# Kernel tuning notes

Measured on AMD Instinct MI355X. Metric: run time of the kernel, lower is better.

The kernel has to match this reference:

```python
import jax, jax.numpy as jnp
import numpy as np

B = 4096
NUM_USERS = 100000
H_DIM = 128          # HIDDEN_DIM
IN_DIM = 128 + 8 + 32  # BOARD_FEAT_DIM + ACTION_BITS + USER_EMB_DIM


def _conv(x, w, b):
    # x: [B,C,H,W], w: [O,I,3,3] (torch OIHW), padding=1 -> SAME
    y = jax.lax.conv_general_dilated(
        x, w, window_strides=(1, 1), padding='SAME',
        dimension_numbers=('NCHW', 'OIHW', 'NCHW'))
    return y + b[None, :, None, None]


def _maxpool2(x):
    return jax.lax.reduce_window(x, -jnp.inf, jax.lax.max,
                                 (1, 1, 2, 2), (1, 1, 2, 2), 'VALID')


def setup_inputs() -> dict:
    key = jax.random.key(0)
    ks = jax.random.split(key, 24)
    f32 = jnp.float32

    def n(k, shape, s=0.05):
        return jax.random.normal(k, shape, dtype=f32) * s

    return {
        'board': jax.random.uniform(ks[0], (B, 1, 32, 32), dtype=f32),
        'h': jax.random.normal(ks[1], (1, B, H_DIM), dtype=f32),
        'action_token': jax.random.randint(ks[2], (B,), 0, 256, dtype=jnp.int32),
        'user_idx': jax.random.randint(ks[3], (B,), 0, NUM_USERS, dtype=jnp.int32),
        # SmallBoardCNN params
        'conv1_w': n(ks[4], (16, 1, 3, 3)), 'conv1_b': n(ks[5], (16,)),
        'conv2_w': n(ks[6], (32, 16, 3, 3)), 'conv2_b': n(ks[7], (32,)),
        'conv3_w': n(ks[8], (64, 32, 3, 3)), 'conv3_b': n(ks[9], (64,)),
        'conv4_w': n(ks[10], (128, 64, 3, 3)), 'conv4_b': n(ks[11], (128,)),
        'proj_w': n(ks[12], (128, 128)), 'proj_b': n(ks[13], (128,)),
        # user embedding
        'emb': n(ks[14], (NUM_USERS, 32), 1.0),
        # GRU params (torch layout: [3H, in], gate order r,z,n)
        'w_ih': n(ks[15], (3 * H_DIM, IN_DIM)), 'w_hh': n(ks[16], (3 * H_DIM, H_DIM)),
        'b_ih': n(ks[17], (3 * H_DIM,)), 'b_hh': n(ks[18], (3 * H_DIM,)),
        # head
        'head_w': n(ks[19], (6, H_DIM)), 'head_b': n(ks[20], (6,)),
    }


def reference(board, h, action_token, user_idx,
              conv1_w, conv1_b, conv2_w, conv2_b, conv3_w, conv3_b,
              conv4_w, conv4_b, proj_w, proj_b, emb,
              w_ih, w_hh, b_ih, b_hh, head_w, head_b):
    # SmallBoardCNN
    x = jax.nn.relu(_conv(board, conv1_w, conv1_b))
    x = jax.nn.relu(_conv(x, conv2_w, conv2_b))
    x = _maxpool2(x)                       # [B,32,16,16]
    x = jax.nn.relu(_conv(x, conv3_w, conv3_b))
    x = _maxpool2(x)                       # [B,64,8,8]
    x = jax.nn.relu(_conv(x, conv4_w, conv4_b))
    bf = x.mean(axis=(2, 3)) @ proj_w.T + proj_b   # AdaptiveAvgPool(1,1) + Linear -> [B,128]

    # int_to_8bits, batched
    abits = ((action_token[:, None] >> jnp.arange(8)) & 1).astype(jnp.float32)  # [B,8]
    uemb = emb[user_idx]                              # [B,32]
    xin = jnp.concatenate([bf, abits, uemb], axis=1)  # [B,168]

    # single GRU step (torch GRUCell math, gate order r,z,n)
    h0 = h[0]                                         # [B,128]
    gi = xin @ w_ih.T + b_ih                          # [B,384]
    gh = h0 @ w_hh.T + b_hh
    r = jax.nn.sigmoid(gi[:, :H_DIM] + gh[:, :H_DIM])
    z = jax.nn.sigmoid(gi[:, H_DIM:2 * H_DIM] + gh[:, H_DIM:2 * H_DIM])
    n_ = jnp.tanh(gi[:, 2 * H_DIM:] + r * gh[:, 2 * H_DIM:])
    h_new = (1.0 - z) * n_ + z * h0                   # [B,128]

    logits = h_new @ head_w.T + head_b                # [B,6]
    return logits, h_new[None]                        # h_new: [1,B,128]
```

## Files before the change

### kernel.cpp

```cpp
#include <hip/hip_runtime.h>
#include <hip/hip_bf16.h>

#define BATCH 4096

typedef __attribute__((ext_vector_type(8))) short short8;
typedef __attribute__((ext_vector_type(16))) float f32x16;

#define WB1_ELEM 0
#define WB2_ELEM 512
#define WB3_ELEM 5120
#define WB4_ELEM 23552
#define WB_TOTAL 97280

#define A1_OFF 2320
#define ZS1_OFF 35088
#define A2_OFF 35152
#define ZS2_OFF 51536
#define SMEM_F 51600
#define ZS3_REL 8192
#define MEANV_OFF 8320

static __device__ __forceinline__ unsigned pack2(float a, float b) {
    __hip_bfloat16 lo = __float2bfloat16(a), hi = __float2bfloat16(b);
    unsigned short ul = *(unsigned short*)&lo, uh = *(unsigned short*)&hi;
    return ((unsigned)uh << 16) | ul;
}

static __device__ __forceinline__ void store_bf16(void* p, float v) {
    __hip_bfloat16 b = __float2bfloat16(v);
    *(unsigned short*)p = *(unsigned short*)&b;
}

__global__ void prepack_weights(const float* __restrict__ w1,
                                const float* __restrict__ w2,
                                const float* __restrict__ w3,
                                const float* __restrict__ w4,
                                __hip_bfloat16* __restrict__ wb) {
    int g = blockIdx.x * 256 + threadIdx.x;
    if (g < 512) {
        int oc = g >> 4, k = g & 15;
        float v = (oc < 16 && k < 9) ? w1[oc * 9 + k] : 0.f;
        wb[g] = __float2bfloat16(v);
    } else if (g < WB3_ELEM) {
        int gg = g - WB2_ELEM;
        int oc = gg / 144, r = gg - oc * 144, tap = r >> 4, ic = r & 15;
        wb[g] = __float2bfloat16(w2[oc * 144 + ic * 9 + tap]);
    } else if (g < WB4_ELEM) {
        int gg = g - WB3_ELEM;
        int oc = gg / 288, r = gg - oc * 288, tap = r >> 5, ic = r & 31;
        wb[g] = __float2bfloat16(w3[oc * 288 + ic * 9 + tap]);
    } else if (g < WB_TOTAL) {
        int gg = g - WB4_ELEM;
        int oc = gg / 576, r = gg - oc * 576, tap = r >> 6, ic = r & 63;
        wb[g] = __float2bfloat16(w4[oc * 576 + ic * 9 + tap]);
    }
}

__global__ __launch_bounds__(256, 3) void cnn_fused_kernel(
    const float* __restrict__ board,
    const float* __restrict__ b1, const float* __restrict__ b2,
    const float* __restrict__ b3, const float* __restrict__ b4,
    const float* __restrict__ pw, const float* __restrict__ pb,
    const __hip_bfloat16* __restrict__ wb,
    float* __restrict__ bf_out)
{
    __shared__ alignas(16) char smem[SMEM_F];
    unsigned short* sbu = (unsigned short*)smem;
    char* a1b = smem + A1_OFF;
    char* a3b = smem;
    float* meanv = (float*)(smem + MEANV_OFF);

    const int t = threadIdx.x;
    const int img = blockIdx.x;
    const int w = t >> 6;
    const int l = t & 63;
    const int n = l & 31;
    const int h = l >> 5;

    const char* wb3 = (const char*)(wb + WB3_ELEM);
    const char* wb4 = (const char*)(wb + WB4_ELEM);

    {
        for (int i = t; i < 132; i += 256) {
            int row, col;
            if (i < 34)       { row = 0;  col = i; }
            else if (i < 68)  { row = 33; col = i - 34; }
            else if (i < 100) { row = i - 68 + 1;  col = 0; }
            else              { row = i - 100 + 1; col = 33; }
            sbu[row * 34 + col] = 0;
        }
        uint4 z; z.x = z.y = z.z = z.w = 0u;
        if (t < 4) ((uint4*)(smem + ZS1_OFF))[t] = z;
        else if (t >= 4 && t < 8) ((uint4*)(smem + ZS2_OFF))[t - 4] = z;
    }
    __syncthreads();

    {
        float4 v = ((const float4*)board)[img * 256 + t];
        const int p0 = t * 4;
        const int row = (p0 >> 5) + 1, col = (p0 & 31) + 1;
        unsigned short* d = sbu + row * 34 + col;
        __hip_bfloat16 x0 = __float2bfloat16(v.x), x1 = __float2bfloat16(v.y);
        __hip_bfloat16 x2 = __float2bfloat16(v.z), x3 = __float2bfloat16(v.w);
        d[0] = *(unsigned short*)&x0; d[1] = *(unsigned short*)&x1;
        d[2] = *(unsigned short*)&x2; d[3] = *(unsigned short*)&x3;
    }
    __syncthreads();

    {
        const short8 A1 = *(const short8*)((const char*)wb + (n * 16 + h * 8) * 2);
        float b1s[8];
#pragma unroll
        for (int r = 0; r < 8; ++r) b1s[r] = b1[(r & 3) + 8 * (r >> 2) + 4 * h];
        const unsigned* sbw = (const unsigned*)smem;
#pragma unroll 1
        for (int yi = 0; yi < 8; ++yi) {
            const int y = 8 * w + yi;
            unsigned short c[3][3];
#pragma unroll
            for (int dy = 0; dy < 3; ++dy) {
                const int base = (y + dy) * 17 + (n >> 1);
                const unsigned w0 = sbw[base], w1v = sbw[base + 1];
                if (n & 1) {
                    c[dy][0] = (unsigned short)(w0 >> 16);
                    c[dy][1] = (unsigned short)(w1v & 0xffff);
                    c[dy][2] = (unsigned short)(w1v >> 16);
                } else {
                    c[dy][0] = (unsigned short)(w0 & 0xffff);
                    c[dy][1] = (unsigned short)(w0 >> 16);
                    c[dy][2] = (unsigned short)(w1v & 0xffff);
                }
            }
            short8 Bv;
            if (h == 0) {
                Bv[0] = (short)c[0][0]; Bv[1] = (short)c[0][1]; Bv[2] = (short)c[0][2];
                Bv[3] = (short)c[1][0]; Bv[4] = (short)c[1][1]; Bv[5] = (short)c[1][2];
                Bv[6] = (short)c[2][0]; Bv[7] = (short)c[2][1];
            } else {
                Bv = (short8)0;
                Bv[0] = (short)c[2][2];
            }
            f32x16 acc = __builtin_amdgcn_mfma_f32_32x32x16_bf16(A1, Bv, (f32x16)0.0f, 0, 0, 0);
            float v8[8];
#pragma unroll
            for (int r = 0; r < 8; ++r) v8[r] = fmaxf(acc[r] + b1s[r], 0.f);
            const int key = ((n >> 2) & 1) << 4;
            char* dst = a1b + (y * 32 + n) * 32;
            uint2 u0, u1;
            u0.x = pack2(v8[0], v8[1]); u0.y = pack2(v8[2], v8[3]);
            u1.x = pack2(v8[4], v8[5]); u1.y = pack2(v8[6], v8[7]);
            *(uint2*)(dst + ((h * 8) ^ key)) = u0;
            *(uint2*)(dst + ((h * 8 + 16) ^ key)) = u1;
        }
    }
    __syncthreads();

    {
        const char* wb2 = (const char*)(wb + WB2_ELEM);
        short8 Bw[9];
#pragma unroll
        for (int tp = 0; tp < 9; ++tp)
            Bw[tp] = *(const short8*)(wb2 + (n * 144 + tp * 16 + h * 8) * 2);
        const float biasv = b2[n];
        const int y_off = 2 * ((n >> 2) & 1) + ((n >> 1) & 1);
        const int x_off = 2 * ((n >> 3) & 3) + (n & 1);

#pragma unroll 1
        for (int pp = 0; pp < 2; ++pp) {
            const int py_base = 4 * w + 2 * pp;
            const int yb = 2 * py_base + y_off;
#pragma unroll 1
            for (int pxh = 0; pxh < 2; ++pxh) {
                const int x0 = 16 * pxh + x_off;
                f32x16 acc0 = (f32x16)0.0f, acc1 = (f32x16)0.0f;
#pragma unroll
                for (int tp = 0; tp < 9; ++tp) {
                    const int dy = tp / 3, dx = tp - 3 * dy;
                    const int r_u = yb + dy - 1;
                    const int c0 = x0 + dx - 1, c1 = x0 + 8 + dx - 1;
                    const bool okr = (unsigned)r_u < 32u;
                    const int off0 = (okr && (unsigned)c0 < 32u)
                        ? (A1_OFF + (r_u * 32 + c0) * 32 + ((h * 16) ^ (((c0 >> 2) & 1) << 4)))
                        : (ZS1_OFF + h * 16);
                    const int off1 = (okr && (unsigned)c1 < 32u)
                        ? (A1_OFF + (r_u * 32 + c1) * 32 + ((h * 16) ^ (((c1 >> 2) & 1) << 4)))
                        : (ZS1_OFF + h * 16);
                    short8 A0 = *(const short8*)(smem + off0);
                    short8 A1v = *(const short8*)(smem + off1);
                    acc0 = __builtin_amdgcn_mfma_f32_32x32x16_bf16(A0, Bw[tp], acc0, 0, 0, 0);
                    acc1 = __builtin_amdgcn_mfma_f32_32x32x16_bf16(A1v, Bw[tp], acc1, 0, 0, 0);
                }
                const int py = py_base + h;
#pragma unroll
                for (int e = 0; e < 2; ++e) {
                    const f32x16 acc = e ? acc1 : acc0;
                    const int pxb = 2 * pxh + e;
#pragma unroll
                    for (int j = 0; j < 4; ++j) {
                        float v = fmaxf(fmaxf(acc[4 * j], acc[4 * j + 1]),
                                        fmaxf(acc[4 * j + 2], acc[4 * j + 3]));
                        v = fmaxf(v + biasv, 0.f);
                        const int px = 4 * pxb + j;
                        const int key = (py + 2 * px) & 3;
                        store_bf16(smem + A2_OFF + (py * 16 + px) * 64 +
                                   ((((n >> 3) ^ key) & 3) << 4) + ((n * 2) & 15), v);
                    }
                }
            }
        }
    }
    __syncthreads();

    {
        uint4 z; z.x = z.y = z.z = z.w = 0u;
        if (t < 8) ((uint4*)(a3b + ZS3_REL))[t] = z;
    }
    __syncthreads();

    {
        const int y_off = 2 * ((n >> 2) & 1) + ((n >> 1) & 1);
        const int x_off = 2 * ((n >> 3) & 3) + (n & 1);
        const int y_in = 4 * w + y_off;
        f32x16 acc00 = (f32x16)0.0f, acc01 = (f32x16)0.0f;
        f32x16 acc10 = (f32x16)0.0f, acc11 = (f32x16)0.0f;
#pragma unroll
        for (int step = 0; step < 18; ++step) {
            const int tp = step >> 1, kh = step & 1;
            const int dy = tp / 3, dx = tp - 3 * dy;
            short8 B0 = *(const short8*)(wb3 + ((n)      * 288 + tp * 32 + kh * 16 + h * 8) * 2);
            short8 B1 = *(const short8*)(wb3 + ((32 + n) * 288 + tp * 32 + kh * 16 + h * 8) * 2);
            const int row_u = y_in + dy - 1;
            const int col0 = x_off + dx - 1;
            const int col1 = col0 + 8;
            const int sbase = kh * 32 + h * 16;
            const bool okr = (unsigned)row_u < 16u;
            const int off0 = (okr && (unsigned)col0 < 16u)
                ? (A2_OFF + row_u * 1024 + col0 * 64 + (sbase ^ (((row_u + 2 * col0) & 3) << 4)))
                : (ZS2_OFF + sbase);
            const int off1 = (okr && (unsigned)col1 < 16u)
                ? (A2_OFF + row_u * 1024 + col1 * 64 + (sbase ^ (((row_u + 2 * col1) & 3) << 4)))
                : (ZS2_OFF + sbase);
            short8 A0 = *(const short8*)(smem + off0);
            short8 A1v = *(const short8*)(smem + off1);
            acc00 = __builtin_amdgcn_mfma_f32_32x32x16_bf16(A0, B0, acc00, 0, 0, 0);
            acc01 = __builtin_amdgcn_mfma_f32_32x32x16_bf16(A0, B1, acc01, 0, 0, 0);
            acc10 = __builtin_amdgcn_mfma_f32_32x32x16_bf16(A1v, B0, acc10, 0, 0, 0);
            acc11 = __builtin_amdgcn_mfma_f32_32x32x16_bf16(A1v, B1, acc11, 0, 0, 0);
        }
        const int py = 2 * w + h;
#pragma unroll
        for (int e = 0; e < 4; ++e) {
            const f32x16 acc = (e == 0) ? acc00 : (e == 1) ? acc01 : (e == 2) ? acc10 : acc11;
            const int pxb = e >> 1, ocb = e & 1;
            const float biasv = b3[32 * ocb + n];
#pragma unroll
            for (int j = 0; j < 4; ++j) {
                float v = fmaxf(fmaxf(acc[4 * j], acc[4 * j + 1]),
                                fmaxf(acc[4 * j + 2], acc[4 * j + 3]));
                v = fmaxf(v + biasv, 0.f);
                const int px = 4 * pxb + j;
                const int byte_in = ocb * 64 + n * 2;
                const int key3 = (py + 2 * px) & 7;
                store_bf16(a3b + (py * 8 + px) * 128 +
                           ((((byte_in >> 4) ^ key3) << 4) | (byte_in & 15)), v);
            }
        }
    }
    __syncthreads();

    {
        const int x4 = n & 7, y4 = (n >> 3) & 3;
        f32x16 aE0 = (f32x16)0.0f, aO0 = (f32x16)0.0f;
        f32x16 aE1 = (f32x16)0.0f, aO1 = (f32x16)0.0f;
#pragma unroll
        for (int dy = 0; dy < 3; ++dy)
#pragma unroll
            for (int dx = 0; dx < 3; ++dx) {
                const int row0 = y4 + dy - 1;
                const int col_u = x4 + dx - 1;
                const bool okc = (unsigned)col_u < 8u;
                const bool ok0 = okc && ((unsigned)row0 < 8u);
                const bool ok1 = okc && ((unsigned)(row0 + 4) < 8u);
#pragma unroll
                for (int kc = 0; kc < 4; ++kc) {
                    const int s4 = kc * 32 + h * 16;
                    const int off0 = ok0
                        ? ((row0 * 8 + col_u) * 128 + (s4 ^ (((row0 + 2 * col_u) & 7) << 4)))
                        : (ZS3_REL + s4);
                    const int off1 = ok1
                        ? (((row0 + 4) * 8 + col_u) * 128 + (s4 ^ (((row0 + 4 + 2 * col_u) & 7) << 4)))
                        : (ZS3_REL + s4);
                    short8 B = *(const short8*)(wb4 + ((32 * w + n) * 576 + (dy * 3 + dx) * 64 + kc * 16 + h * 8) * 2);
                    short8 A0 = *(const short8*)(a3b + off0);
                    short8 A1v = *(const short8*)(a3b + off1);
                    if (kc & 1) {
                        aO0 = __builtin_amdgcn_mfma_f32_32x32x16_bf16(A0, B, aO0, 0, 0, 0);
                        aO1 = __builtin_amdgcn_mfma_f32_32x32x16_bf16(A1v, B, aO1, 0, 0, 0);
                    } else {
                        aE0 = __builtin_amdgcn_mfma_f32_32x32x16_bf16(A0, B, aE0, 0, 0, 0);
                        aE1 = __builtin_amdgcn_mfma_f32_32x32x16_bf16(A1v, B, aE1, 0, 0, 0);
                    }
                }
            }
        const float biasv = b4[32 * w + n];
        float s = 0.f;
#pragma unroll
        for (int r = 0; r < 16; ++r) {
            s += fmaxf(aE0[r] + aO0[r] + biasv, 0.f);
            s += fmaxf(aE1[r] + aO1[r] + biasv, 0.f);
        }
        s += __shfl_xor(s, 32);
        if (l < 32) meanv[32 * w + l] = s * (1.f / 64.f);
    }
    __syncthreads();

    if (t < 128) {
        float acc = pb[t];
        const float* wrow = pw + t * 128;
        for (int k = 0; k < 128; ++k) acc = fmaf(meanv[k], wrow[k], acc);
        bf_out[img * 128 + t] = acc;
    }
}

__global__ __launch_bounds__(384) void gru_kernel(
    const float* __restrict__ hin,
    const int* __restrict__ atok, const int* __restrict__ uidx,
    const float* __restrict__ emb,
    const float* __restrict__ w_ih, const float* __restrict__ w_hh,
    const float* __restrict__ b_ih, const float* __restrict__ b_hh,
    const float* __restrict__ head_w, const float* __restrict__ head_b,
    float* __restrict__ out)
{
    const int img0 = blockIdx.x * 8;
    const int t = threadIdx.x;
    __shared__ float xin_s[8][168];
    __shared__ float h0_s[8][128];
    __shared__ float gis[8][384];
    __shared__ float ghs[8][384];
    __shared__ float hn_s[8][128];
    const float* bf = out + BATCH * 6;

    for (int idx = t; idx < 8 * 168; idx += 384) {
        const int r = idx / 168, k = idx - r * 168;
        const int row = img0 + r;
        float v;
        if (k < 128)      v = bf[row * 128 + k];
        else if (k < 136) v = (float)((atok[row] >> (k - 128)) & 1);
        else              v = emb[uidx[row] * 32 + (k - 136)];
        xin_s[r][k] = v;
    }
    for (int idx = t; idx < 8 * 128; idx += 384) {
        const int r = idx >> 7, k = idx & 127;
        h0_s[r][k] = hin[(img0 + r) * 128 + k];
    }
    __syncthreads();

    {
        const int o = t;
        float gi[8], gh[8];
        const float bi = b_ih[o], bh = b_hh[o];
#pragma unroll
        for (int r = 0; r < 8; ++r) { gi[r] = bi; gh[r] = bh; }
        const float* wi = w_ih + o * 168;
        const float* wh = w_hh + o * 128;
        for (int k = 0; k < 128; ++k) {
            const float wv = wi[k];
            const float wvh = wh[k];
#pragma unroll
            for (int r = 0; r < 8; ++r) {
                gi[r] = fmaf(wv, xin_s[r][k], gi[r]);
                gh[r] = fmaf(wvh, h0_s[r][k], gh[r]);
            }
        }
        for (int k = 128; k < 168; ++k) {
            const float wv = wi[k];
#pragma unroll
            for (int r = 0; r < 8; ++r) gi[r] = fmaf(wv, xin_s[r][k], gi[r]);
        }
#pragma unroll
        for (int r = 0; r < 8; ++r) { gis[r][o] = gi[r]; ghs[r][o] = gh[r]; }
    }
    __syncthreads();

    if (t < 128) {
#pragma unroll
        for (int r = 0; r < 8; ++r) {
            const float rg = 1.f / (1.f + expf(-(gis[r][t] + ghs[r][t])));
            const float z  = 1.f / (1.f + expf(-(gis[r][128 + t] + ghs[r][128 + t])));
            const float nn = tanhf(gis[r][256 + t] + rg * ghs[r][256 + t]);
            const float hn = (1.f - z) * nn + z * h0_s[r][t];
            hn_s[r][t] = hn;
            out[BATCH * 6 + (img0 + r) * 128 + t] = hn;
        }
    }
    __syncthreads();

    if (t < 48) {
        const int r = t / 6, j = t - r * 6;
        float acc = head_b[j];
        const float* wrow = head_w + j * 128;
        for (int k = 0; k < 128; ++k) acc = fmaf(hn_s[r][k], wrow[k], acc);
        out[(img0 + r) * 6 + j] = acc;
    }
}

extern "C" void kernel_launch(void* const* d_in, const int* in_sizes, int n_in,
                              void* d_out, int out_size, void* d_ws, size_t ws_size,
                              hipStream_t stream) {
    const float* board = (const float*)d_in[0];
    const float* h     = (const float*)d_in[1];
    const int*   atok  = (const int*)d_in[2];
    const int*   uidx  = (const int*)d_in[3];
    const float* w1 = (const float*)d_in[4];
    const float* b1 = (const float*)d_in[5];
    const float* w2 = (const float*)d_in[6];
    const float* b2 = (const float*)d_in[7];
    const float* w3 = (const float*)d_in[8];
    const float* b3 = (const float*)d_in[9];
    const float* w4 = (const float*)d_in[10];
    const float* b4 = (const float*)d_in[11];
    const float* pw = (const float*)d_in[12];
    const float* pb = (const float*)d_in[13];
    const float* emb  = (const float*)d_in[14];
    const float* w_ih = (const float*)d_in[15];
    const float* w_hh = (const float*)d_in[16];
    const float* b_ih = (const float*)d_in[17];
    const float* b_hh = (const float*)d_in[18];
    const float* head_w = (const float*)d_in[19];
    const float* head_b = (const float*)d_in[20];
    float* out = (float*)d_out;
    __hip_bfloat16* wb = (__hip_bfloat16*)d_ws;

    float* bf = out + BATCH * 6;
    prepack_weights<<<(WB_TOTAL + 255) / 256, 256, 0, stream>>>(w1, w2, w3, w4, wb);
    cnn_fused_kernel<<<BATCH, 256, 0, stream>>>(board, b1, b2, b3, b4,
                                                pw, pb, wb, bf);
    gru_kernel<<<BATCH / 8, 384, 0, stream>>>(h, atok, uidx, emb, w_ih, w_hh,
                                              b_ih, b_hh, head_w, head_b, out);
}
```

Baseline: 213.8 us.

## Double CNN block to 512 threads and split conv work across eight waves

The fused CNN kernel now runs 512 threads (8 waves) per image instead of 256. Each conv stage is repartitioned so every wave does half the previous work: conv1 rows, conv2 pooled rows, conv3 split by pixel half, and conv4 split by row half with partial means combined in shared memory. The projection dot product is split across two threads per output and joined with a shuffle. The goal is more waves to hide latency and a shorter serial chain per wave. The cost is fewer accumulators per wave and lost register reuse: conv2 weights are now reloaded inside the loop, and conv3/conv4 A/B fragments are no longer shared across two MFMAs. The 512x6 launch bounds also tighten the register budget.

```diff
diff --git a/kernel.cpp b/kernel.cpp
--- a/kernel.cpp
+++ b/kernel.cpp
@@ -19,6 +19,7 @@
 #define SMEM_F 51600
 #define ZS3_REL 8192
 #define MEANV_OFF 8320
+#define MEANP_OFF 8832
 
 static __device__ __forceinline__ unsigned pack2(float a, float b) {
     __hip_bfloat16 lo = __float2bfloat16(a), hi = __float2bfloat16(b);
@@ -56,7 +57,7 @@
     }
 }
 
-__global__ __launch_bounds__(256, 3) void cnn_fused_kernel(
+__global__ __launch_bounds__(512, 6) void cnn_fused_kernel(
     const float* __restrict__ board,
     const float* __restrict__ b1, const float* __restrict__ b2,
     const float* __restrict__ b3, const float* __restrict__ b4,
@@ -69,6 +70,7 @@
     char* a1b = smem + A1_OFF;
     char* a3b = smem;
     float* meanv = (float*)(smem + MEANV_OFF);
+    float* meanp = (float*)(smem + MEANP_OFF);
 
     const int t = threadIdx.x;
     const int img = blockIdx.x;
@@ -81,8 +83,8 @@
     const char* wb4 = (const char*)(wb + WB4_ELEM);
 
     {
-        for (int i = t; i < 132; i += 256) {
-            int row, col;
+        if (t < 132) {
+            int i = t, row, col;
             if (i < 34)       { row = 0;  col = i; }
             else if (i < 68)  { row = 33; col = i - 34; }
             else if (i < 100) { row = i - 68 + 1;  col = 0; }
@@ -90,20 +92,18 @@
             sbu[row * 34 + col] = 0;
         }
         uint4 z; z.x = z.y = z.z = z.w = 0u;
-        if (t < 4) ((uint4*)(smem + ZS1_OFF))[t] = z;
-        else if (t >= 4 && t < 8) ((uint4*)(smem + ZS2_OFF))[t - 4] = z;
-    }
-    __syncthreads();
-
-    {
-        float4 v = ((const float4*)board)[img * 256 + t];
-        const int p0 = t * 4;
+        if (t >= 256 && t < 260) ((uint4*)(smem + ZS1_OFF))[t - 256] = z;
+        else if (t >= 260 && t < 264) ((uint4*)(smem + ZS2_OFF))[t - 260] = z;
+    }
+    __syncthreads();
+
+    {
+        float2 v = ((const float2*)board)[img * 512 + t];
+        const int p0 = t * 2;
         const int row = (p0 >> 5) + 1, col = (p0 & 31) + 1;
         unsigned short* d = sbu + row * 34 + col;
         __hip_bfloat16 x0 = __float2bfloat16(v.x), x1 = __float2bfloat16(v.y);
-        __hip_bfloat16 x2 = __float2bfloat16(v.z), x3 = __float2bfloat16(v.w);
         d[0] = *(unsigned short*)&x0; d[1] = *(unsigned short*)&x1;
-        d[2] = *(unsigned short*)&x2; d[3] = *(unsigned short*)&x3;
     }
     __syncthreads();
 
@@ -114,8 +114,8 @@
         for (int r = 0; r < 8; ++r) b1s[r] = b1[(r & 3) + 8 * (r >> 2) + 4 * h];
         const unsigned* sbw = (const unsigned*)smem;
 #pragma unroll 1
-        for (int yi = 0; yi < 8; ++yi) {
-            const int y = 8 * w + yi;
+        for (int yi = 0; yi < 4; ++yi) {
+            const int y = 4 * w + yi;
             unsigned short c[3][3];
 #pragma unroll
             for (int dy = 0; dy < 3; ++dy) {
@@ -157,54 +157,48 @@
 
     {
         const char* wb2 = (const char*)(wb + WB2_ELEM);
-        short8 Bw[9];
-#pragma unroll
-        for (int tp = 0; tp < 9; ++tp)
-            Bw[tp] = *(const short8*)(wb2 + (n * 144 + tp * 16 + h * 8) * 2);
         const float biasv = b2[n];
         const int y_off = 2 * ((n >> 2) & 1) + ((n >> 1) & 1);
         const int x_off = 2 * ((n >> 3) & 3) + (n & 1);
+        const int py_base = 2 * w;
+        const int yb = 4 * w + y_off;
 
 #pragma unroll 1
-        for (int pp = 0; pp < 2; ++pp) {
-            const int py_base = 4 * w + 2 * pp;
-            const int yb = 2 * py_base + y_off;
-#pragma unroll 1
-            for (int pxh = 0; pxh < 2; ++pxh) {
-                const int x0 = 16 * pxh + x_off;
-                f32x16 acc0 = (f32x16)0.0f, acc1 = (f32x16)0.0f;
-#pragma unroll
-                for (int tp = 0; tp < 9; ++tp) {
-                    const int dy = tp / 3, dx = tp - 3 * dy;
-                    const int r_u = yb + dy - 1;
-                    const int c0 = x0 + dx - 1, c1 = x0 + 8 + dx - 1;
-                    const bool okr = (unsigned)r_u < 32u;
-                    const int off0 = (okr && (unsigned)c0 < 32u)
-                        ? (A1_OFF + (r_u * 32 + c0) * 32 + ((h * 16) ^ (((c0 >> 2) & 1) << 4)))
-                        : (ZS1_OFF + h * 16);
-                    const int off1 = (okr && (unsigned)c1 < 32u)
-                        ? (A1_OFF + (r_u * 32 + c1) * 32 + ((h * 16) ^ (((c1 >> 2) & 1) << 4)))
-                        : (ZS1_OFF + h * 16);
-                    short8 A0 = *(const short8*)(smem + off0);
-                    short8 A1v = *(const short8*)(smem + off1);
-                    acc0 = __builtin_amdgcn_mfma_f32_32x32x16_bf16(A0, Bw[tp], acc0, 0, 0, 0);
-                    acc1 = __builtin_amdgcn_mfma_f32_32x32x16_bf16(A1v, Bw[tp], acc1, 0, 0, 0);
-                }
-                const int py = py_base + h;
-#pragma unroll
-                for (int e = 0; e < 2; ++e) {
-                    const f32x16 acc = e ? acc1 : acc0;
-                    const int pxb = 2 * pxh + e;
-#pragma unroll
-                    for (int j = 0; j < 4; ++j) {
-                        float v = fmaxf(fmaxf(acc[4 * j], acc[4 * j + 1]),
-                                        fmaxf(acc[4 * j + 2], acc[4 * j + 3]));
-                        v = fmaxf(v + biasv, 0.f);
-                        const int px = 4 * pxb + j;
-                        const int key = (py + 2 * px) & 3;
-                        store_bf16(smem + A2_OFF + (py * 16 + px) * 64 +
-                                   ((((n >> 3) ^ key) & 3) << 4) + ((n * 2) & 15), v);
-                    }
+        for (int pxh = 0; pxh < 2; ++pxh) {
+            const int x0 = 16 * pxh + x_off;
+            f32x16 acc0 = (f32x16)0.0f, acc1 = (f32x16)0.0f;
+#pragma unroll
+            for (int tp = 0; tp < 9; ++tp) {
+                const int dy = tp / 3, dx = tp - 3 * dy;
+                short8 Bw = *(const short8*)(wb2 + (n * 144 + tp * 16 + h * 8) * 2);
+                const int r_u = yb + dy - 1;
+                const int c0 = x0 + dx - 1, c1 = x0 + 8 + dx - 1;
+                const bool okr = (unsigned)r_u < 32u;
+                const int off0 = (okr && (unsigned)c0 < 32u)
+                    ? (A1_OFF + (r_u * 32 + c0) * 32 + ((h * 16) ^ (((c0 >> 2) & 1) << 4)))
+                    : (ZS1_OFF + h * 16);
+                const int off1 = (okr && (unsigned)c1 < 32u)
+                    ? (A1_OFF + (r_u * 32 + c1) * 32 + ((h * 16) ^ (((c1 >> 2) & 1) << 4)))
+                    : (ZS1_OFF + h * 16);
+                short8 A0 = *(const short8*)(smem + off0);
+                short8 A1v = *(const short8*)(smem + off1);
+                acc0 = __builtin_amdgcn_mfma_f32_32x32x16_bf16(A0, Bw, acc0, 0, 0, 0);
+                acc1 = __builtin_amdgcn_mfma_f32_32x32x16_bf16(A1v, Bw, acc1, 0, 0, 0);
+            }
+            const int py = py_base + h;
+#pragma unroll
+            for (int e = 0; e < 2; ++e) {
+                const f32x16 acc = e ? acc1 : acc0;
+                const int pxb = 2 * pxh + e;
+#pragma unroll
+                for (int j = 0; j < 4; ++j) {
+                    float v = fmaxf(fmaxf(acc[4 * j], acc[4 * j + 1]),
+                                    fmaxf(acc[4 * j + 2], acc[4 * j + 3]));
+                    v = fmaxf(v + biasv, 0.f);
+                    const int px = 4 * pxb + j;
+                    const int key = (py + 2 * px) & 3;
+                    store_bf16(smem + A2_OFF + (py * 16 + px) * 64 +
+                               ((((n >> 3) ^ key) & 3) << 4) + ((n * 2) & 15), v);
                 }
             }
         }
@@ -218,11 +212,12 @@
     __syncthreads();
 
     {
+        const int rg = w >> 1;
+        const int pxh = w & 1;
         const int y_off = 2 * ((n >> 2) & 1) + ((n >> 1) & 1);
-        const int x_off = 2 * ((n >> 3) & 3) + (n & 1);
-        const int y_in = 4 * w + y_off;
-        f32x16 acc00 = (f32x16)0.0f, acc01 = (f32x16)0.0f;
-        f32x16 acc10 = (f32x16)0.0f, acc11 = (f32x16)0.0f;
+        const int x_off = 2 * ((n >> 3) & 3) + (n & 1) + 8 * pxh;
+        const int y_in = 4 * rg + y_off;
+        f32x16 acc0 = (f32x16)0.0f, acc1 = (f32x16)0.0f;
 #pragma unroll
         for (int step = 0; step < 18; ++step) {
             const int tp = step >> 1, kh = step & 1;
@@ -230,36 +225,28 @@
             short8 B0 = *(const short8*)(wb3 + ((n)      * 288 + tp * 32 + kh * 16 + h * 8) * 2);
             short8 B1 = *(const short8*)(wb3 + ((32 + n) * 288 + tp * 32 + kh * 16 + h * 8) * 2);
             const int row_u = y_in + dy - 1;
-            const int col0 = x_off + dx - 1;
-            const int col1 = col0 + 8;
+            const int col_u = x_off + dx - 1;
             const int sbase = kh * 32 + h * 16;
-            const bool okr = (unsigned)row_u < 16u;
-            const int off0 = (okr && (unsigned)col0 < 16u)
-                ? (A2_OFF + row_u * 1024 + col0 * 64 + (sbase ^ (((row_u + 2 * col0) & 3) << 4)))
+            const bool ok = ((unsigned)row_u < 16u) && ((unsigned)col_u < 16u);
+            const int off = ok
+                ? (A2_OFF + row_u * 1024 + col_u * 64 + (sbase ^ (((row_u + 2 * col_u) & 3) << 4)))
                 : (ZS2_OFF + sbase);
-            const int off1 = (okr && (unsigned)col1 < 16u)
-                ? (A2_OFF + row_u * 1024 + col1 * 64 + (sbase ^ (((row_u + 2 * col1) & 3) << 4)))
-                : (ZS2_OFF + sbase);
-            short8 A0 = *(const short8*)(smem + off0);
-            short8 A1v = *(const short8*)(smem + off1);
-            acc00 = __builtin_amdgcn_mfma_f32_32x32x16_bf16(A0, B0, acc00, 0, 0, 0);
-            acc01 = __builtin_amdgcn_mfma_f32_32x32x16_bf16(A0, B1, acc01, 0, 0, 0);
-            acc10 = __builtin_amdgcn_mfma_f32_32x32x16_bf16(A1v, B0, acc10, 0, 0, 0);
-            acc11 = __builtin_amdgcn_mfma_f32_32x32x16_bf16(A1v, B1, acc11, 0, 0, 0);
-        }
-        const int py = 2 * w + h;
-#pragma unroll
-        for (int e = 0; e < 4; ++e) {
-            const f32x16 acc = (e == 0) ? acc00 : (e == 1) ? acc01 : (e == 2) ? acc10 : acc11;
-            const int pxb = e >> 1, ocb = e & 1;
-            const float biasv = b3[32 * ocb + n];
+            short8 A0 = *(const short8*)(smem + off);
+            acc0 = __builtin_amdgcn_mfma_f32_32x32x16_bf16(A0, B0, acc0, 0, 0, 0);
+            acc1 = __builtin_amdgcn_mfma_f32_32x32x16_bf16(A0, B1, acc1, 0, 0, 0);
+        }
+        const int py = 2 * rg + h;
+#pragma unroll
+        for (int e = 0; e < 2; ++e) {
+            const f32x16 acc = e ? acc1 : acc0;
+            const float biasv = b3[32 * e + n];
 #pragma unroll
             for (int j = 0; j < 4; ++j) {
                 float v = fmaxf(fmaxf(acc[4 * j], acc[4 * j + 1]),
                                 fmaxf(acc[4 * j + 2], acc[4 * j + 3]));
                 v = fmaxf(v + biasv, 0.f);
-                const int px = 4 * pxb + j;
-                const int byte_in = ocb * 64 + n * 2;
+                const int px = 4 * pxh + j;
+                const int byte_in = e * 64 + n * 2;
                 const int key3 = (py + 2 * px) & 7;
                 store_bf16(a3b + (py * 8 + px) * 128 +
                            ((((byte_in >> 4) ^ key3) << 4) | (byte_in & 15)), v);
@@ -269,56 +256,48 @@
     __syncthreads();
 
     {
+        const int ocb4 = w >> 1;
+        const int mt = w & 1;
         const int x4 = n & 7, y4 = (n >> 3) & 3;
-        f32x16 aE0 = (f32x16)0.0f, aO0 = (f32x16)0.0f;
-        f32x16 aE1 = (f32x16)0.0f, aO1 = (f32x16)0.0f;
+        f32x16 a0 = (f32x16)0.0f;
 #pragma unroll
         for (int dy = 0; dy < 3; ++dy)
 #pragma unroll
             for (int dx = 0; dx < 3; ++dx) {
-                const int row0 = y4 + dy - 1;
+                const int row_m = 4 * mt + y4 + dy - 1;
                 const int col_u = x4 + dx - 1;
-                const bool okc = (unsigned)col_u < 8u;
-                const bool ok0 = okc && ((unsigned)row0 < 8u);
-                const bool ok1 = okc && ((unsigned)(row0 + 4) < 8u);
+                const bool ok = ((unsigned)col_u < 8u) && ((unsigned)row_m < 8u);
 #pragma unroll
                 for (int kc = 0; kc < 4; ++kc) {
                     const int s4 = kc * 32 + h * 16;
-                    const int off0 = ok0
-                        ? ((row0 * 8 + col_u) * 128 + (s4 ^ (((row0 + 2 * col_u) & 7) << 4)))
+                    const int off = ok
+                        ? ((row_m * 8 + col_u) * 128 + (s4 ^ (((row_m + 2 * col_u) & 7) << 4)))
                         : (ZS3_REL + s4);
-                    const int off1 = ok1
-                        ? (((row0 + 4) * 8 + col_u) * 128 + (s4 ^ (((row0 + 4 + 2 * col_u) & 7) << 4)))
-                        : (ZS3_REL + s4);
-                    short8 B = *(const short8*)(wb4 + ((32 * w + n) * 576 + (dy * 3 + dx) * 64 + kc * 16 + h * 8) * 2);
-                    short8 A0 = *(const short8*)(a3b + off0);
-                    short8 A1v = *(const short8*)(a3b + off1);
-                    if (kc & 1) {
-                        aO0 = __builtin_amdgcn_mfma_f32_32x32x16_bf16(A0, B, aO0, 0, 0, 0);
-                        aO1 = __builtin_amdgcn_mfma_f32_32x32x16_bf16(A1v, B, aO1, 0, 0, 0);
-                    } else {
-                        aE0 = __builtin_amdgcn_mfma_f32_32x32x16_bf16(A0, B, aE0, 0, 0, 0);
-                        aE1 = __builtin_amdgcn_mfma_f32_32x32x16_bf16(A1v, B, aE1, 0, 0, 0);
-                    }
+                    short8 B = *(const short8*)(wb4 + ((32 * ocb4 + n) * 576 + (dy * 3 + dx) * 64 + kc * 16 + h * 8) * 2);
+                    short8 A0 = *(const short8*)(a3b + off);
+                    a0 = __builtin_amdgcn_mfma_f32_32x32x16_bf16(A0, B, a0, 0, 0, 0);
                 }
             }
-        const float biasv = b4[32 * w + n];
+        const float biasv = b4[32 * ocb4 + n];
         float s = 0.f;
 #pragma unroll
-        for (int r = 0; r < 16; ++r) {
-            s += fmaxf(aE0[r] + aO0[r] + biasv, 0.f);
-            s += fmaxf(aE1[r] + aO1[r] + biasv, 0.f);
-        }
+        for (int r = 0; r < 16; ++r) s += fmaxf(a0[r] + biasv, 0.f);
         s += __shfl_xor(s, 32);
-        if (l < 32) meanv[32 * w + l] = s * (1.f / 64.f);
-    }
-    __syncthreads();
-
-    if (t < 128) {
-        float acc = pb[t];
-        const float* wrow = pw + t * 128;
-        for (int k = 0; k < 128; ++k) acc = fmaf(meanv[k], wrow[k], acc);
-        bf_out[img * 128 + t] = acc;
+        if (l < 32) meanp[mt * 128 + 32 * ocb4 + l] = s;
+    }
+    __syncthreads();
+
+    if (t < 128) meanv[t] = (meanp[t] + meanp[128 + t]) * (1.f / 64.f);
+    __syncthreads();
+
+    if (t < 256) {
+        const int o = t >> 1, kh = t & 1;
+        const float* wrow = pw + o * 128 + kh * 64;
+        const float* mv = meanv + kh * 64;
+        float acc = 0.f;
+        for (int k = 0; k < 64; ++k) acc = fmaf(mv[k], wrow[k], acc);
+        acc += __shfl_xor(acc, 1);
+        if (kh == 0) bf_out[img * 128 + o] = acc + pb[o];
     }
 }
 
@@ -433,7 +412,7 @@
 
     float* bf = out + BATCH * 6;
     prepack_weights<<<(WB_TOTAL + 255) / 256, 256, 0, stream>>>(w1, w2, w3, w4, wb);
-    cnn_fused_kernel<<<BATCH, 256, 0, stream>>>(board, b1, b2, b3, b4,
+    cnn_fused_kernel<<<BATCH, 512, 0, stream>>>(board, b1, b2, b3, b4,
                                                 pw, pb, wb, bf);
     gru_kernel<<<BATCH / 8, 384, 0, stream>>>(h, atok, uidx, emb, w_ih, w_hh,
                                               b_ih, b_hh, head_w, head_b, out);
```

Measured after the change: 380.8 us. +78.1%, slower.

## Band conv1/conv2 into two row halves to shrink LDS and raise occupancy

Applied to the files above, without the earlier changes.

Conv1 output is now produced in two row bands of 17 rows each (with halo) instead of the full 32x32 map, and each band is consumed by conv2 before the next band is computed. This cuts the conv1 activation buffer roughly in half, so shared memory per block drops and launch bounds are raised from 3 to 4 blocks per CU. The projection GEMV is also split across all 256 threads, two per output joined with a shuffle. The cost is extra barriers per band and recomputing one halo row of conv1 per band.

```diff
diff --git a/kernel.cpp b/kernel.cpp
--- a/kernel.cpp
+++ b/kernel.cpp
@@ -13,10 +13,10 @@
 #define WB_TOTAL 97280
 
 #define A1_OFF 2320
-#define ZS1_OFF 35088
-#define A2_OFF 35152
-#define ZS2_OFF 51536
-#define SMEM_F 51600
+#define ZS1_OFF 19728
+#define A2_OFF 19792
+#define ZS2_OFF 36176
+#define SMEM_F 36240
 #define ZS3_REL 8192
 #define MEANV_OFF 8320
 
@@ -56,7 +56,7 @@
     }
 }
 
-__global__ __launch_bounds__(256, 3) void cnn_fused_kernel(
+__global__ __launch_bounds__(256, 4) void cnn_fused_kernel(
     const float* __restrict__ board,
     const float* __restrict__ b1, const float* __restrict__ b2,
     const float* __restrict__ b3, const float* __restrict__ b4,
@@ -81,8 +81,8 @@
     const char* wb4 = (const char*)(wb + WB4_ELEM);
 
     {
-        for (int i = t; i < 132; i += 256) {
-            int row, col;
+        if (t < 132) {
+            int i = t, row, col;
             if (i < 34)       { row = 0;  col = i; }
             else if (i < 68)  { row = 33; col = i - 34; }
             else if (i < 100) { row = i - 68 + 1;  col = 0; }
@@ -90,8 +90,8 @@
             sbu[row * 34 + col] = 0;
         }
         uint4 z; z.x = z.y = z.z = z.w = 0u;
-        if (t < 4) ((uint4*)(smem + ZS1_OFF))[t] = z;
-        else if (t >= 4 && t < 8) ((uint4*)(smem + ZS2_OFF))[t - 4] = z;
+        if (t >= 136 && t < 140) ((uint4*)(smem + ZS1_OFF))[t - 136] = z;
+        else if (t >= 140 && t < 144) ((uint4*)(smem + ZS2_OFF))[t - 140] = z;
     }
     __syncthreads();
 
@@ -107,68 +107,71 @@
     }
     __syncthreads();
 
-    {
-        const short8 A1 = *(const short8*)((const char*)wb + (n * 16 + h * 8) * 2);
-        float b1s[8];
-#pragma unroll
-        for (int r = 0; r < 8; ++r) b1s[r] = b1[(r & 3) + 8 * (r >> 2) + 4 * h];
-        const unsigned* sbw = (const unsigned*)smem;
 #pragma unroll 1
-        for (int yi = 0; yi < 8; ++yi) {
-            const int y = 8 * w + yi;
-            unsigned short c[3][3];
-#pragma unroll
-            for (int dy = 0; dy < 3; ++dy) {
-                const int base = (y + dy) * 17 + (n >> 1);
-                const unsigned w0 = sbw[base], w1v = sbw[base + 1];
-                if (n & 1) {
-                    c[dy][0] = (unsigned short)(w0 >> 16);
-                    c[dy][1] = (unsigned short)(w1v & 0xffff);
-                    c[dy][2] = (unsigned short)(w1v >> 16);
+    for (int band = 0; band < 2; ++band) {
+        const int base = band * 15;
+
+        {
+            const short8 A1 = *(const short8*)((const char*)wb + (n * 16 + h * 8) * 2);
+            float b1s[8];
+#pragma unroll
+            for (int r = 0; r < 8; ++r) b1s[r] = b1[(r & 3) + 8 * (r >> 2) + 4 * h];
+            const unsigned* sbw = (const unsigned*)smem;
+#pragma unroll 1
+            for (int yi = 0; yi < 5; ++yi) {
+                if (yi == 4 && w != 0) break;
+                const int yg = (yi < 4) ? (base + 4 * w + yi) : (base + 16);
+                unsigned short c[3][3];
+#pragma unroll
+                for (int dy = 0; dy < 3; ++dy) {
+                    const int sbase = (yg + dy) * 17 + (n >> 1);
+                    const unsigned w0 = sbw[sbase], w1v = sbw[sbase + 1];
+                    if (n & 1) {
+                        c[dy][0] = (unsigned short)(w0 >> 16);
+                        c[dy][1] = (unsigned short)(w1v & 0xffff);
+                        c[dy][2] = (unsigned short)(w1v >> 16);
+                    } else {
+                        c[dy][0] = (unsigned short)(w0 & 0xffff);
+                        c[dy][1] = (unsigned short)(w0 >> 16);
+                        c[dy][2] = (unsigned short)(w1v & 0xffff);
+                    }
+                }
+                short8 Bv;
+                if (h == 0) {
+                    Bv[0] = (short)c[0][0]; Bv[1] = (short)c[0][1]; Bv[2] = (short)c[0][2];
+                    Bv[3] = (short)c[1][0]; Bv[4] = (short)c[1][1]; Bv[5] = (short)c[1][2];
+                    Bv[6] = (short)c[2][0]; Bv[7] = (short)c[2][1];
                 } else {
-                    c[dy][0] = (unsigned short)(w0 & 0xffff);
-                    c[dy][1] = (unsigned short)(w0 >> 16);
-                    c[dy][2] = (unsigned short)(w1v & 0xffff);
+                    Bv = (short8)0;
+                    Bv[0] = (short)c[2][2];
                 }
+                f32x16 acc = __builtin_amdgcn_mfma_f32_32x32x16_bf16(A1, Bv, (f32x16)0.0f, 0, 0, 0);
+                float v8[8];
+#pragma unroll
+                for (int r = 0; r < 8; ++r) v8[r] = fmaxf(acc[r] + b1s[r], 0.f);
+                const int key = ((n >> 2) & 1) << 4;
+                char* dst = a1b + ((yg - base) * 32 + n) * 32;
+                uint2 u0, u1;
+                u0.x = pack2(v8[0], v8[1]); u0.y = pack2(v8[2], v8[3]);
+                u1.x = pack2(v8[4], v8[5]); u1.y = pack2(v8[6], v8[7]);
+                *(uint2*)(dst + ((h * 8) ^ key)) = u0;
+                *(uint2*)(dst + ((h * 8 + 16) ^ key)) = u1;
             }
-            short8 Bv;
-            if (h == 0) {
-                Bv[0] = (short)c[0][0]; Bv[1] = (short)c[0][1]; Bv[2] = (short)c[0][2];
-                Bv[3] = (short)c[1][0]; Bv[4] = (short)c[1][1]; Bv[5] = (short)c[1][2];
-                Bv[6] = (short)c[2][0]; Bv[7] = (short)c[2][1];
-            } else {
-                Bv = (short8)0;
-                Bv[0] = (short)c[2][2];
-            }
-            f32x16 acc = __builtin_amdgcn_mfma_f32_32x32x16_bf16(A1, Bv, (f32x16)0.0f, 0, 0, 0);
-            float v8[8];
-#pragma unroll
-            for (int r = 0; r < 8; ++r) v8[r] = fmaxf(acc[r] + b1s[r], 0.f);
-            const int key = ((n >> 2) & 1) << 4;
-            char* dst = a1b + (y * 32 + n) * 32;
-            uint2 u0, u1;
-            u0.x = pack2(v8[0], v8[1]); u0.y = pack2(v8[2], v8[3]);
-            u1.x = pack2(v8[4], v8[5]); u1.y = pack2(v8[6], v8[7]);
-            *(uint2*)(dst + ((h * 8) ^ key)) = u0;
-            *(uint2*)(dst + ((h * 8 + 16) ^ key)) = u1;
-        }
-    }
-    __syncthreads();
-
-    {
-        const char* wb2 = (const char*)(wb + WB2_ELEM);
-        short8 Bw[9];
-#pragma unroll
-        for (int tp = 0; tp < 9; ++tp)
-            Bw[tp] = *(const short8*)(wb2 + (n * 144 + tp * 16 + h * 8) * 2);
-        const float biasv = b2[n];
-        const int y_off = 2 * ((n >> 2) & 1) + ((n >> 1) & 1);
-        const int x_off = 2 * ((n >> 3) & 3) + (n & 1);
-
-#pragma unroll 1
-        for (int pp = 0; pp < 2; ++pp) {
-            const int py_base = 4 * w + 2 * pp;
-            const int yb = 2 * py_base + y_off;
+        }
+        __syncthreads();
+
+        {
+            const char* wb2 = (const char*)(wb + WB2_ELEM);
+            short8 Bw[9];
+#pragma unroll
+            for (int tp = 0; tp < 9; ++tp)
+                Bw[tp] = *(const short8*)(wb2 + (n * 144 + tp * 16 + h * 8) * 2);
+            const float biasv = b2[n];
+            const int y_off = 2 * ((n >> 2) & 1) + ((n >> 1) & 1);
+            const int x_off = 2 * ((n >> 3) & 3) + (n & 1);
+            const int py_base = 8 * band + 2 * w;
+            const int yb = 16 * band + 4 * w + y_off;
+
 #pragma unroll 1
             for (int pxh = 0; pxh < 2; ++pxh) {
                 const int x0 = 16 * pxh + x_off;
@@ -176,14 +179,14 @@
 #pragma unroll
                 for (int tp = 0; tp < 9; ++tp) {
                     const int dy = tp / 3, dx = tp - 3 * dy;
-                    const int r_u = yb + dy - 1;
+                    const int lr = yb + dy - 1 - base;
                     const int c0 = x0 + dx - 1, c1 = x0 + 8 + dx - 1;
-                    const bool okr = (unsigned)r_u < 32u;
+                    const bool okr = (unsigned)lr < 17u;
                     const int off0 = (okr && (unsigned)c0 < 32u)
-                        ? (A1_OFF + (r_u * 32 + c0) * 32 + ((h * 16) ^ (((c0 >> 2) & 1) << 4)))
+                        ? (A1_OFF + (lr * 32 + c0) * 32 + ((h * 16) ^ (((c0 >> 2) & 1) << 4)))
                         : (ZS1_OFF + h * 16);
                     const int off1 = (okr && (unsigned)c1 < 32u)
-                        ? (A1_OFF + (r_u * 32 + c1) * 32 + ((h * 16) ^ (((c1 >> 2) & 1) << 4)))
+                        ? (A1_OFF + (lr * 32 + c1) * 32 + ((h * 16) ^ (((c1 >> 2) & 1) << 4)))
                         : (ZS1_OFF + h * 16);
                     short8 A0 = *(const short8*)(smem + off0);
                     short8 A1v = *(const short8*)(smem + off1);
@@ -208,8 +211,8 @@
                 }
             }
         }
-    }
-    __syncthreads();
+        __syncthreads();
+    }
 
     {
         uint4 z; z.x = z.y = z.z = z.w = 0u;
@@ -314,11 +317,14 @@
     }
     __syncthreads();
 
-    if (t < 128) {
-        float acc = pb[t];
-        const float* wrow = pw + t * 128;
-        for (int k = 0; k < 128; ++k) acc = fmaf(meanv[k], wrow[k], acc);
-        bf_out[img * 128 + t] = acc;
+    {
+        const int o = t >> 1, kh = t & 1;
+        const float* wrow = pw + o * 128 + kh * 64;
+        const float* mv = meanv + kh * 64;
+        float acc = 0.f;
+        for (int k = 0; k < 64; ++k) acc = fmaf(mv[k], wrow[k], acc);
+        acc += __shfl_xor(acc, 1);
+        if (kh == 0) bf_out[img * 128 + o] = acc + pb[o];
     }
 }
 
```

Measured after the change: 214.8 us. Within noise of the previous version (+0.5%).
